# Kernel tuning notes

Hardware: AMD Instinct MI355X
Metric: run time of the kernel (lower is better)

The kernel has to match this reference:

```python
import jax, jax.numpy as jnp
import numpy as np

B, T, C, H = 512, 4096, 7, 3  # batch, time, 7 classes, 3 heads


def setup_inputs() -> dict:
    key = jax.random.key(0)
    k0, k1, k2, k3, k4, k5 = jax.random.split(key, 6)
    # outputs are treated as probabilities (log is taken directly); keep them in (0.01, 1]
    mk_out = lambda k: jax.random.uniform(k, (B, T, C), dtype=jnp.float32, minval=0.01, maxval=1.0)
    return {
        "out0": mk_out(k0),
        "out1": mk_out(k1),
        "out2": mk_out(k2),
        "labels_3": jax.random.randint(k3, (B, T, H), 0, C, dtype=jnp.int64),
        "mask": jax.random.uniform(k4, (B, T), dtype=jnp.float32),
        "reward": jax.random.uniform(k5, (B, T, H), dtype=jnp.float32),
    }


def reference(out0, out1, out2, labels_3, mask, reward):
    N = B * T
    outs = jnp.stack([out0, out1, out2], axis=0).reshape(H, N, C)   # [3, N, 7]
    labels = labels_3.reshape(N, H).T                               # [3, N]
    rw = reward.reshape(N, H).T                                     # [3, N]
    valid = mask.reshape(N) < 0.5                                   # [N] bool
    n_valid = valid.sum()

    # gather probability of the true class per head: op[h, n] = outs[h, n, labels[h, n]]
    op = jnp.take_along_axis(outs, labels[:, :, None], axis=2)[..., 0]  # [3, N]
    # original: sum_h -dot(log(op_h), sr_h) / n_valid  (n_valid identical across heads)
    loss = -jnp.where(valid[None, :], jnp.log(op) * rw, 0.0).sum() / n_valid

    pred = jnp.argmax(outs, axis=-1)                                # [3, N]
    correct = jnp.all(pred == labels, axis=0) & valid               # product over heads on valid positions
    n_correct = correct.sum()
    return loss, n_correct, n_valid
```

## Files before the change

kernel.cpp:

```cpp
#include <hip/hip_runtime.h>

constexpr long long N_ROWS = 512LL * 4096LL;
constexpr int BLOCK  = 256;
constexpr int CHUNK  = 256;
constexpr int NBLOCKS = 2048;
constexpr int NCHUNKS_TOTAL   = (int)(N_ROWS / CHUNK);
constexpr int CHUNKS_PER_BLOCK = NCHUNKS_TOTAL / NBLOCKS;


__device__ __forceinline__ void async_copy16(const void* g, void* l) {
    __builtin_amdgcn_global_load_lds(
        (const __attribute__((address_space(1))) unsigned int*)g,
        (__attribute__((address_space(3))) unsigned int*)l,
        16, 0, 0);
}

__global__ __launch_bounds__(BLOCK) void shortloss_main(
    const float* __restrict__ out0,
    const float* __restrict__ out1,
    const float* __restrict__ out2,
    const int*   __restrict__ labels,
    const float* __restrict__ mask,
    const float* __restrict__ reward,
    float4*      __restrict__ partials)
{
    __shared__ float lds[7168];
    float* lds_out = lds;
    int*   lds_lab = (int*)(lds + 5376);
    float* lds_rw  = lds + 6144;
    float* lds_msk = lds + 6912;

    const int tid = threadIdx.x;
    const float* outs[3] = {out0, out1, out2};

    float loss_local = 0.0f;
    int   ccount = 0, vcount = 0;

    for (int k = 0; k < CHUNKS_PER_BLOCK; ++k) {
        const long long c    = (long long)k * NBLOCKS + blockIdx.x;
        const long long row0 = c * CHUNK;

        #pragma unroll
        for (int h = 0; h < 3; ++h) {
            const float* src = outs[h] + row0 * 7;
            float*       dst = lds_out + h * 1792;
            async_copy16(src + (size_t)tid * 4, dst + tid * 4);
            if (tid < 192)
                async_copy16(src + (size_t)(256 + tid) * 4, dst + (256 + tid) * 4);
        }
        if (tid < 192) {
            async_copy16(labels + row0 * 3 + (size_t)tid * 4, lds_lab + tid * 4);
            async_copy16(reward + row0 * 3 + (size_t)tid * 4, lds_rw  + tid * 4);
        }
        if (tid < 64) {
            async_copy16(mask + row0 + (size_t)tid * 4, lds_msk + tid * 4);
        }
        __syncthreads();

        const bool valid = lds_msk[tid] < 0.5f;
        vcount += valid ? 1 : 0;

        int lab[3], h_ok = 1;
        float rw[3];
        #pragma unroll
        for (int h = 0; h < 3; ++h) {
            lab[h] = lds_lab[tid * 3 + h];
            rw[h]  = lds_rw [tid * 3 + h];
        }

        float lsum = 0.0f;
        #pragma unroll
        for (int h = 0; h < 3; ++h) {
            const float* vr = lds_out + h * 1792 + tid * 7;
            float v[7];
            #pragma unroll
            for (int cc = 0; cc < 7; ++cc) v[cc] = vr[cc];

            float best = v[0]; int bestc = 0;
            #pragma unroll
            for (int cc = 1; cc < 7; ++cc)
                if (v[cc] > best) { best = v[cc]; bestc = cc; }

            float opv = v[0];
            #pragma unroll
            for (int cc = 1; cc < 7; ++cc)
                opv = (lab[h] == cc) ? v[cc] : opv;

            lsum += __logf(opv) * rw[h];
            h_ok &= (bestc == lab[h]) ? 1 : 0;
        }
        loss_local += valid ? lsum : 0.0f;
        ccount     += (valid && h_ok) ? 1 : 0;

        __syncthreads();
    }

    float L = loss_local;
    int   C = ccount, V = vcount;
    #pragma unroll
    for (int off = 32; off > 0; off >>= 1) {
        L += __shfl_down(L, off, 64);
        C += __shfl_down(C, off, 64);
        V += __shfl_down(V, off, 64);
    }

    __shared__ float sL[BLOCK / 64];
    __shared__ int   sC[BLOCK / 64], sV[BLOCK / 64];
    const int wave = tid >> 6;
    if ((tid & 63) == 0) { sL[wave] = L; sC[wave] = C; sV[wave] = V; }
    __syncthreads();
    if (tid == 0) {
        float l = 0.0f; int cc = 0, vv = 0;
        #pragma unroll
        for (int w = 0; w < BLOCK / 64; ++w) { l += sL[w]; cc += sC[w]; vv += sV[w]; }
        partials[blockIdx.x] = make_float4(l, (float)cc, (float)vv, 0.0f);
    }
}

__global__ __launch_bounds__(256) void shortloss_reduce(
    const float4* __restrict__ partials,
    float* __restrict__ out)
{
    float L = 0.0f, C = 0.0f, V = 0.0f;
    for (int i = threadIdx.x; i < NBLOCKS; i += 256) {
        float4 p = partials[i];
        L += p.x; C += p.y; V += p.z;
    }
    #pragma unroll
    for (int off = 32; off > 0; off >>= 1) {
        L += __shfl_down(L, off, 64);
        C += __shfl_down(C, off, 64);
        V += __shfl_down(V, off, 64);
    }
    __shared__ float sL[4], sC[4], sV[4];
    const int wave = threadIdx.x >> 6;
    if ((threadIdx.x & 63) == 0) { sL[wave] = L; sC[wave] = C; sV[wave] = V; }
    __syncthreads();
    if (threadIdx.x == 0) {
        float l = 0.0f, c = 0.0f, v = 0.0f;
        #pragma unroll
        for (int w = 0; w < 4; ++w) { l += sL[w]; c += sC[w]; v += sV[w]; }
        out[0] = -l / v;
        out[1] = c;
        out[2] = v;
    }
}

extern "C" void kernel_launch(void* const* d_in, const int* in_sizes, int n_in,
                              void* d_out, int out_size, void* d_ws, size_t ws_size,
                              hipStream_t stream) {
    const float* out0   = (const float*)d_in[0];
    const float* out1   = (const float*)d_in[1];
    const float* out2   = (const float*)d_in[2];
    const int*   labels = (const int*)  d_in[3];
    const float* mask   = (const float*)d_in[4];
    const float* reward = (const float*)d_in[5];

    float4* partials = (float4*)d_ws;

    shortloss_main<<<NBLOCKS, BLOCK, 0, stream>>>(
        out0, out1, out2, labels, mask, reward, partials);
    shortloss_reduce<<<1, 256, 0, stream>>>(partials, (float*)d_out);
}
```

Baseline: 227.7 us.

## Double-buffer LDS staging and give each block contiguous chunks

Each block now takes a contiguous run of 4 chunks instead of chunks strided across the grid. Loads go through two LDS buffers: the async global-to-LDS copy for the next chunk is issued before computing on the current one, so memory traffic can overlap with the per-row argmax, log and reduction work. The cost is double the LDS per block, which may cut how many blocks fit on a CU. The overlap may also be lost if the compiler inserts a full vmcnt wait before the LDS reads.

```diff
diff --git a/kernel.cpp b/kernel.cpp
--- a/kernel.cpp
+++ b/kernel.cpp
@@ -1,14 +1,14 @@
 #include <hip/hip_runtime.h>
 
 constexpr long long N_ROWS = 512LL * 4096LL;
-constexpr int BLOCK  = 256;
-constexpr int CHUNK  = 256;
-constexpr int NBLOCKS = 2048;
-constexpr int NCHUNKS_TOTAL   = (int)(N_ROWS / CHUNK);
-constexpr int CHUNKS_PER_BLOCK = NCHUNKS_TOTAL / NBLOCKS;
+constexpr int BLOCK   = 256;
+constexpr int CHUNK   = 256;
+constexpr int CPB     = 4;
+constexpr int NBLOCKS = (int)(N_ROWS / ((long long)CHUNK * CPB));
 
+constexpr int BUF_WORDS = 7168;
 
-__device__ __forceinline__ void async_copy16(const void* g, void* l) {
+__device__ __forceinline__ void async16(const float* g, float* l) {
     __builtin_amdgcn_global_load_lds(
         (const __attribute__((address_space(1))) unsigned int*)g,
         (__attribute__((address_space(3))) unsigned int*)l,
@@ -24,54 +24,43 @@
     const float* __restrict__ reward,
     float4*      __restrict__ partials)
 {
-    __shared__ float lds[7168];
-    float* lds_out = lds;
-    int*   lds_lab = (int*)(lds + 5376);
-    float* lds_rw  = lds + 6144;
-    float* lds_msk = lds + 6912;
-
+    __shared__ float lds[2 * BUF_WORDS];
     const int tid = threadIdx.x;
+    const long long c0 = (long long)blockIdx.x * CPB;
     const float* outs[3] = {out0, out1, out2};
 
-    float loss_local = 0.0f;
-    int   ccount = 0, vcount = 0;
-
-    for (int k = 0; k < CHUNKS_PER_BLOCK; ++k) {
-        const long long c    = (long long)k * NBLOCKS + blockIdx.x;
-        const long long row0 = c * CHUNK;
-
+    auto stage = [&](long long c, int b) {
+        float* buf = lds + b * BUF_WORDS;
         #pragma unroll
         for (int h = 0; h < 3; ++h) {
-            const float* src = outs[h] + row0 * 7;
-            float*       dst = lds_out + h * 1792;
-            async_copy16(src + (size_t)tid * 4, dst + tid * 4);
+            const float* src = outs[h] + c * (CHUNK * 7);
+            float*       dst = buf + h * 1792;
+            async16(src + 4 * (size_t)tid, dst + 4 * tid);
             if (tid < 192)
-                async_copy16(src + (size_t)(256 + tid) * 4, dst + (256 + tid) * 4);
+                async16(src + 4 * (size_t)(256 + tid), dst + 4 * (256 + tid));
         }
         if (tid < 192) {
-            async_copy16(labels + row0 * 3 + (size_t)tid * 4, lds_lab + tid * 4);
-            async_copy16(reward + row0 * 3 + (size_t)tid * 4, lds_rw  + tid * 4);
+            async16((const float*)(labels) + c * (CHUNK * 3) + 4 * (size_t)tid, buf + 5376 + 4 * tid);
+            async16(reward + c * (CHUNK * 3) + 4 * (size_t)tid,                 buf + 6144 + 4 * tid);
         }
-        if (tid < 64) {
-            async_copy16(mask + row0 + (size_t)tid * 4, lds_msk + tid * 4);
-        }
-        __syncthreads();
+        if (tid < 64)
+            async16(mask + c * CHUNK + 4 * (size_t)tid, buf + 6912 + 4 * tid);
+    };
 
-        const bool valid = lds_msk[tid] < 0.5f;
-        vcount += valid ? 1 : 0;
+    float L = 0.0f;
+    int   C = 0, V = 0;
 
-        int lab[3], h_ok = 1;
-        float rw[3];
-        #pragma unroll
-        for (int h = 0; h < 3; ++h) {
-            lab[h] = lds_lab[tid * 3 + h];
-            rw[h]  = lds_rw [tid * 3 + h];
-        }
-
+    auto compute = [&](int b) {
+        const float* buf  = lds + b * BUF_WORDS;
+        const int*   labp = (const int*)(buf + 5376);
+        const bool valid = buf[6912 + tid] < 0.5f;
+        V += valid ? 1 : 0;
+        int   ok   = 1;
         float lsum = 0.0f;
         #pragma unroll
         for (int h = 0; h < 3; ++h) {
-            const float* vr = lds_out + h * 1792 + tid * 7;
+            const int lbl = labp[tid * 3 + h];
+            const float* vr = buf + h * 1792 + tid * 7;
             float v[7];
             #pragma unroll
             for (int cc = 0; cc < 7; ++cc) v[cc] = vr[cc];
@@ -84,26 +73,30 @@
             float opv = v[0];
             #pragma unroll
             for (int cc = 1; cc < 7; ++cc)
-                opv = (lab[h] == cc) ? v[cc] : opv;
+                opv = (lbl == cc) ? v[cc] : opv;
 
-            lsum += __logf(opv) * rw[h];
-            h_ok &= (bestc == lab[h]) ? 1 : 0;
+            lsum += __logf(opv) * buf[6144 + tid * 3 + h];
+            ok &= (bestc == lbl) ? 1 : 0;
         }
-        loss_local += valid ? lsum : 0.0f;
-        ccount     += (valid && h_ok) ? 1 : 0;
+        L += valid ? lsum : 0.0f;
+        C += (valid && ok) ? 1 : 0;
+    };
 
+    stage(c0, 0);
+    __syncthreads();
+    #pragma unroll
+    for (int k = 0; k < CPB; ++k) {
+        if (k + 1 < CPB) stage(c0 + k + 1, (k + 1) & 1);
+        compute(k & 1);
         __syncthreads();
     }
 
-    float L = loss_local;
-    int   C = ccount, V = vcount;
     #pragma unroll
     for (int off = 32; off > 0; off >>= 1) {
         L += __shfl_down(L, off, 64);
         C += __shfl_down(C, off, 64);
         V += __shfl_down(V, off, 64);
     }
-
     __shared__ float sL[BLOCK / 64];
     __shared__ int   sC[BLOCK / 64], sV[BLOCK / 64];
     const int wave = tid >> 6;
```

Result: no change. 226.0 us (-0.7%).
